# Kernel tuning notes

Hardware: AMD Instinct MI355X
Metric: run time of the kernel (lower is better)

Reference implementation:

```python
import jax, jax.numpy as jnp
import numpy as np

H = 16
D_MODEL = 1024
D_K = D_MODEL // H


def setup_inputs() -> dict:
    key = jax.random.key(0)
    ks = jax.random.split(key, 10)
    B, S = 2, 2048
    q = jax.random.normal(ks[0], (B, S, D_MODEL), dtype=jnp.float32)
    k = jax.random.normal(ks[1], (B, S, D_MODEL), dtype=jnp.float32)
    v = jax.random.normal(ks[2], (B, S, D_MODEL), dtype=jnp.float32)
    mask = jax.random.randint(ks[3], (B, 1, S), 0, 2, dtype=jnp.int32)
    s = 1.0 / np.sqrt(D_MODEL)
    w_q = jax.random.normal(ks[4], (D_MODEL, D_MODEL), dtype=jnp.float32) * s
    b_q = jnp.zeros((D_MODEL,), dtype=jnp.float32)
    w_v = jax.random.normal(ks[5], (D_MODEL, D_MODEL), dtype=jnp.float32) * s
    b_v = jnp.zeros((D_MODEL,), dtype=jnp.float32)
    w_o = jax.random.normal(ks[6], (D_MODEL, D_MODEL), dtype=jnp.float32) * s
    b_o = jnp.zeros((D_MODEL,), dtype=jnp.float32)
    return {"q": q, "k": k, "v": v, "mask": mask,
            "w_q": w_q, "b_q": b_q, "w_v": w_v, "b_v": b_v,
            "w_o": w_o, "b_o": b_o}


def _split_heads(x, B):
    # [B, S, D] -> [B, H, S, d_k]
    return x.reshape(B, -1, H, D_K).transpose(0, 2, 1, 3)


def reference(q, k, v, mask, w_q, b_q, w_v, b_v, w_o, b_o):
    B = q.shape[0]
    # NOTE: source uses w_q for BOTH q and k (w_k is dead code) — reproduced faithfully.
    qh = _split_heads(q @ w_q.T + b_q, B)
    kh = _split_heads(k @ w_q.T + b_q, B)
    vh = _split_heads(v @ w_v.T + b_v, B)
    scores = jnp.einsum('bhqd,bhkd->bhqk', qh, kh) * (1.0 / np.sqrt(D_K))
    # mask [B,1,S] -> unsqueeze(1) -> [B,1,1,S], broadcast over heads and query dim
    m = mask[:, None, :, :]
    scores = jnp.where(m == 0, -jnp.inf, scores)
    attn = jax.nn.softmax(scores, axis=-1)  # dropout is identity (eval / p=0)
    out = jnp.einsum('bhqk,bhkd->bhqd', attn, vh)
    out = out.transpose(0, 2, 1, 3).reshape(B, -1, D_MODEL)
    out = out @ w_o.T + b_o
    return out, attn
```

## Files before the change

kernel.cpp:

```cpp
#include <hip/hip_runtime.h>

#define S_LEN 2048
#define DMODEL 1024
#define NH 16
#define DK 64
#define BATCH 2
#define BS (BATCH * S_LEN)
#define KHALF 1024

typedef _Float16 f16;
typedef _Float16 f16x8 __attribute__((ext_vector_type(8)));
typedef _Float16 f16x4 __attribute__((ext_vector_type(4)));
typedef float f32x4 __attribute__((ext_vector_type(4)));

__device__ __forceinline__ f32x4 mfma16(f16x8 a, f16x8 b, f32x4 c) {
  return __builtin_amdgcn_mfma_f32_16x16x32_f16(a, b, c, 0, 0, 0);
}

__global__ __launch_bounds__(256) void cvt6(
    const float* __restrict__ a0, const float* __restrict__ a1,
    const float* __restrict__ a2, const float* __restrict__ a3,
    const float* __restrict__ a4, const float* __restrict__ a5,
    f16* __restrict__ d0, f16* __restrict__ d1, f16* __restrict__ d2,
    f16* __restrict__ d3, f16* __restrict__ d4, f16* __restrict__ d5) {
  const int y = blockIdx.y;
  const float* s;
  f16* d;
  switch (y) {
    case 0: s = a0; d = d0; break;
    case 1: s = a1; d = d1; break;
    case 2: s = a2; d = d2; break;
    case 3: s = a3; d = d3; break;
    case 4: s = a4; d = d4; break;
    default: s = a5; d = d5; break;
  }
  const int n = (y < 3) ? BS * DMODEL : DMODEL * DMODEL;
  const int idx = (blockIdx.x * 256 + threadIdx.x) * 4;
  if (idx >= n) return;
  const float4 v = *reinterpret_cast<const float4*>(&s[idx]);
  f16x4 h = {(f16)v.x, (f16)v.y, (f16)v.z, (f16)v.w};
  *reinterpret_cast<f16x4*>(&d[idx]) = h;
}

template <int MODE>
__device__ __forceinline__ void gemm_body16(const f16* __restrict__ A,
                                            const f16* __restrict__ W,
                                            const float* __restrict__ bias,
                                            void* __restrict__ outp, float scale,
                                            f16 (*As)[72], f16 (*Ws)[72]) {
  const int t = threadIdx.x;
  const int m0 = blockIdx.y * 128;
  const int n0 = blockIdx.x * 128;
  const int wave = t >> 6, lane = t & 63;
  const int wr = wave >> 1, wc = wave & 1;
  const int lcol = lane & 15, kq = lane >> 4;

  f32x4 acc[4][4];
  const f32x4 zero = {0.f, 0.f, 0.f, 0.f};
#pragma unroll
  for (int i = 0; i < 4; ++i)
#pragma unroll
    for (int j = 0; j < 4; ++j) acc[i][j] = zero;

  for (int k0 = 0; k0 < DMODEL; k0 += 64) {
#pragma unroll
    for (int i = 0; i < 4; ++i) {
      const int f = t + i * 256;
      const int r = f >> 3, c = (f & 7) << 3;
      *reinterpret_cast<f16x8*>(&As[r][c]) =
          *reinterpret_cast<const f16x8*>(&A[(size_t)(m0 + r) * DMODEL + k0 + c]);
      *reinterpret_cast<f16x8*>(&Ws[r][c]) =
          *reinterpret_cast<const f16x8*>(&W[(size_t)(n0 + r) * DMODEL + k0 + c]);
    }
    __syncthreads();
#pragma unroll
    for (int ks = 0; ks < 2; ++ks) {
      f16x8 af[4], bf[4];
#pragma unroll
      for (int fr = 0; fr < 4; ++fr)
        af[fr] = *reinterpret_cast<const f16x8*>(
            &As[wr * 64 + fr * 16 + lcol][ks * 32 + kq * 8]);
#pragma unroll
      for (int fc = 0; fc < 4; ++fc)
        bf[fc] = *reinterpret_cast<const f16x8*>(
            &Ws[wc * 64 + fc * 16 + lcol][ks * 32 + kq * 8]);
#pragma unroll
      for (int fr = 0; fr < 4; ++fr)
#pragma unroll
        for (int fc = 0; fc < 4; ++fc)
          acc[fr][fc] = mfma16(af[fr], bf[fc], acc[fr][fc]);
    }
    __syncthreads();
  }

#pragma unroll
  for (int fc = 0; fc < 4; ++fc) {
    const int gj = n0 + wc * 64 + fc * 16 + lcol;
    const float bv = bias[gj];
#pragma unroll
    for (int fr = 0; fr < 4; ++fr) {
#pragma unroll
      for (int r = 0; r < 4; ++r) {
        const int gi = m0 + wr * 64 + fr * 16 + kq * 4 + r;
        const float val = (acc[fr][fc][r] + bv) * scale;
        if constexpr (MODE == 0) {
          const int b = gi >> 11, s = gi & 2047, h = gj >> 6, dk = gj & 63;
          ((f16*)outp)[(((size_t)(b * NH + h) * S_LEN) + s) * DK + dk] = (f16)val;
        } else if constexpr (MODE == 1) {
          const int b = gi >> 11, s = gi & 2047, h = gj >> 6, dk = gj & 63;
          ((f16*)outp)[(((size_t)(b * NH + h) * DK) + dk) * S_LEN + s] = (f16)val;
        } else {
          ((float*)outp)[(size_t)gi * DMODEL + gj] = val;
        }
      }
    }
  }
}

__global__ __launch_bounds__(256, 3) void qkv_gemm(
    const f16* __restrict__ qf, const f16* __restrict__ kf,
    const f16* __restrict__ vf, const f16* __restrict__ wq,
    const float* __restrict__ b_q, const f16* __restrict__ wv,
    const float* __restrict__ b_v, f16* __restrict__ qh, f16* __restrict__ kh,
    f16* __restrict__ vhT) {
  __shared__ f16 As[128][72];
  __shared__ f16 Ws[128][72];
  if (blockIdx.z == 0)
    gemm_body16<0>(qf, wq, b_q, qh, 0.125f, As, Ws);
  else if (blockIdx.z == 1)
    gemm_body16<0>(kf, wq, b_q, kh, 1.0f, As, Ws);
  else
    gemm_body16<1>(vf, wv, b_v, vhT, 1.0f, As, Ws);
}

__global__ __launch_bounds__(256, 2) void gemm_out(const f16* __restrict__ A,
                                                   const f16* __restrict__ W,
                                                   const float* __restrict__ bias,
                                                   float* __restrict__ outp) {
  __shared__ f16 As[128][72];
  __shared__ f16 Ws[128][72];
  gemm_body16<2>(A, W, bias, outp, 1.0f, As, Ws);
}

__global__ __launch_bounds__(256, 4) void attn_fused(
    const f16* __restrict__ qh, const f16* __restrict__ kh,
    const f16* __restrict__ vhT, const int* __restrict__ mask,
    float* __restrict__ attn, f16* __restrict__ ctx) {
  __shared__ __align__(16) unsigned char smem[17920];
  const int t = threadIdx.x;
  const int bh = blockIdx.y, b = bh >> 4, h = bh & 15;
  const int i0 = blockIdx.x * 64;
  const int wave = t >> 6, lane = t & 63;
  const int rh = wave & 1, khf = wave >> 1;
  const int lcol = lane & 15, kq = lane >> 4;
  const int rbase = i0 + rh * 32;
  const int jbase = khf * KHALF;
  float (*Ost)[68] = reinterpret_cast<float(*)[68]>(smem);
  float* lred = reinterpret_cast<float*>(smem + 17408);

  const f16* Q = qh + (size_t)bh * S_LEN * DK;
  const f16* K = kh + (size_t)bh * S_LEN * DK;
  const f16* V = vhT + (size_t)bh * DK * S_LEN;
  const int* msk = mask + b * S_LEN;
  float* Sc = attn + (size_t)bh * S_LEN * S_LEN;

  f16x8 aq[2][2];
#pragma unroll
  for (int rt = 0; rt < 2; ++rt)
#pragma unroll
    for (int ks = 0; ks < 2; ++ks)
      aq[rt][ks] = *reinterpret_cast<const f16x8*>(
          &Q[(size_t)(rbase + rt * 16 + lcol) * DK + ks * 32 + kq * 8]);

  float l_acc[2] = {0.f, 0.f};
  f32x4 o[2][4];
  const f32x4 zero = {0.f, 0.f, 0.f, 0.f};
#pragma unroll
  for (int rt = 0; rt < 2; ++rt)
#pragma unroll
    for (int d = 0; d < 4; ++d) o[rt][d] = zero;

  for (int j0 = jbase; j0 < jbase + KHALF; j0 += 64) {
#pragma unroll
    for (int jh = 0; jh < 2; ++jh) {
      f16x8 ap[2];
#pragma unroll
      for (int jl = 0; jl < 2; ++jl) {
        const int jt = jh * 2 + jl;
        const f16* Krow = &K[(size_t)(j0 + jt * 16 + lcol) * DK + kq * 8];
        const f16x8 bk0 = *reinterpret_cast<const f16x8*>(Krow);
        const f16x8 bk1 = *reinterpret_cast<const f16x8*>(Krow + 32);
        const int4 m4 =
            *reinterpret_cast<const int4*>(&msk[j0 + jt * 16 + kq * 4]);
#pragma unroll
        for (int rt = 0; rt < 2; ++rt) {
          f32x4 c = zero;
          c = mfma16(bk0, aq[rt][0], c);
          c = mfma16(bk1, aq[rt][1], c);
          const float p0 = m4.x ? __expf(c[0]) : 0.f;
          const float p1 = m4.y ? __expf(c[1]) : 0.f;
          const float p2 = m4.z ? __expf(c[2]) : 0.f;
          const float p3 = m4.w ? __expf(c[3]) : 0.f;
          l_acc[rt] += (p0 + p1) + (p2 + p3);
          ap[rt][jl * 4 + 0] = (f16)p0;
          ap[rt][jl * 4 + 1] = (f16)p1;
          ap[rt][jl * 4 + 2] = (f16)p2;
          ap[rt][jl * 4 + 3] = (f16)p3;
        }
      }
#pragma unroll
      for (int d = 0; d < 4; ++d) {
        const f16* Vr =
            &V[(size_t)(d * 16 + lcol) * S_LEN + j0 + jh * 32 + kq * 4];
        const f16x4 v0 = *reinterpret_cast<const f16x4*>(Vr);
        const f16x4 v1 = *reinterpret_cast<const f16x4*>(Vr + 16);
        f16x8 bv;
        bv[0] = v0[0]; bv[1] = v0[1]; bv[2] = v0[2]; bv[3] = v0[3];
        bv[4] = v1[0]; bv[5] = v1[1]; bv[6] = v1[2]; bv[7] = v1[3];
#pragma unroll
        for (int rt = 0; rt < 2; ++rt) o[rt][d] = mfma16(ap[rt], bv, o[rt][d]);
      }
    }
  }

#pragma unroll
  for (int rt = 0; rt < 2; ++rt) {
    float es = l_acc[rt];
    es += __shfl_xor(es, 16);
    es += __shfl_xor(es, 32);
    l_acc[rt] = es;
  }

  if (kq == 0) {
#pragma unroll
    for (int rt = 0; rt < 2; ++rt)
      lred[khf * 64 + rh * 32 + rt * 16 + lcol] = l_acc[rt];
  }
  if (khf == 1) {
#pragma unroll
    for (int rt = 0; rt < 2; ++rt)
#pragma unroll
      for (int d = 0; d < 4; ++d)
#pragma unroll
        for (int r = 0; r < 4; ++r)
          Ost[rh * 32 + rt * 16 + kq * 4 + r][d * 16 + lcol] = o[rt][d][r];
  }
  __syncthreads();

  float ile[2][4];
  float il2[2];
#pragma unroll
  for (int rt = 0; rt < 2; ++rt) {
#pragma unroll
    for (int r = 0; r < 4; ++r) {
      const int rl = rh * 32 + rt * 16 + kq * 4 + r;
      ile[rt][r] = 1.0f / (lred[rl] + lred[64 + rl]);
    }
    const int rl2 = rh * 32 + rt * 16 + lcol;
    il2[rt] = 1.0f / (lred[rl2] + lred[64 + rl2]);
  }

  for (int j0 = jbase; j0 < jbase + KHALF; j0 += 64) {
#pragma unroll
    for (int jt = 0; jt < 4; ++jt) {
      const f16* Krow = &K[(size_t)(j0 + jt * 16 + lcol) * DK + kq * 8];
      const f16x8 bk0 = *reinterpret_cast<const f16x8*>(Krow);
      const f16x8 bk1 = *reinterpret_cast<const f16x8*>(Krow + 32);
      const int4 m4 =
          *reinterpret_cast<const int4*>(&msk[j0 + jt * 16 + kq * 4]);
#pragma unroll
      for (int rt = 0; rt < 2; ++rt) {
        f32x4 c = zero;
        c = mfma16(bk0, aq[rt][0], c);
        c = mfma16(bk1, aq[rt][1], c);
        float4 st;
        st.x = m4.x ? __expf(c[0]) * il2[rt] : 0.f;
        st.y = m4.y ? __expf(c[1]) * il2[rt] : 0.f;
        st.z = m4.z ? __expf(c[2]) * il2[rt] : 0.f;
        st.w = m4.w ? __expf(c[3]) * il2[rt] : 0.f;
        *reinterpret_cast<float4*>(
            &Sc[((size_t)(rbase + rt * 16 + lcol) << 11) + j0 + jt * 16 +
                kq * 4]) = st;
      }
    }
  }

  if (khf == 0) {
#pragma unroll
    for (int rt = 0; rt < 2; ++rt)
#pragma unroll
      for (int d = 0; d < 4; ++d) {
        const int dk = d * 16 + lcol;
#pragma unroll
        for (int r = 0; r < 4; ++r) {
          const int rl = rh * 32 + rt * 16 + kq * 4 + r;
          const float ov = o[rt][d][r] + Ost[rl][dk];
          const int s = rbase + rt * 16 + kq * 4 + r;
          ctx[(size_t)(b * S_LEN + s) * DMODEL + h * DK + dk] =
              (f16)(ov * ile[rt][r]);
        }
      }
  }
}

extern "C" void kernel_launch(void* const* d_in, const int* in_sizes, int n_in,
                              void* d_out, int out_size, void* d_ws, size_t ws_size,
                              hipStream_t stream) {
  const float* q = (const float*)d_in[0];
  const float* k = (const float*)d_in[1];
  const float* v = (const float*)d_in[2];
  const int* mask = (const int*)d_in[3];
  const float* w_q = (const float*)d_in[4];
  const float* b_q = (const float*)d_in[5];
  const float* w_v = (const float*)d_in[6];
  const float* b_v = (const float*)d_in[7];
  const float* w_o = (const float*)d_in[8];
  const float* b_o = (const float*)d_in[9];

  float* out = (float*)d_out;
  float* attn = out + (size_t)BS * DMODEL;

  f16* qf = (f16*)d_ws;
  f16* kf = qf + (size_t)BS * DMODEL;
  f16* vf = kf + (size_t)BS * DMODEL;
  f16* wqf = vf + (size_t)BS * DMODEL;
  f16* wvf = wqf + (size_t)DMODEL * DMODEL;
  f16* wof = wvf + (size_t)DMODEL * DMODEL;
  f16* qh = wof + (size_t)DMODEL * DMODEL;
  f16* kh = qh + (size_t)BS * DMODEL;
  f16* vhT = kh + (size_t)BS * DMODEL;
  f16* ctx = vhT + (size_t)BS * DMODEL;

  cvt6<<<dim3(4096, 6), 256, 0, stream>>>(q, k, v, w_q, w_v, w_o, qf, kf, vf,
                                          wqf, wvf, wof);
  qkv_gemm<<<dim3(8, 32, 3), 256, 0, stream>>>(qf, kf, vf, wqf, b_q, wvf, b_v,
                                               qh, kh, vhT);
  attn_fused<<<dim3(32, 32), 256, 0, stream>>>(qh, kh, vhT, mask, attn, ctx);
  gemm_out<<<dim3(8, 32), 256, 0, stream>>>(ctx, wof, b_o, out);
}
```

Baseline: 1.035 ms.

## Stage K and V tiles through LDS in the fused attention kernel

The attention kernel now loads each 64-key tile of K and V, for both key halves, cooperatively into shared memory, with barriers around each load. The waves then read their MFMA operands from LDS instead of each wave issuing its own strided global loads. This cuts redundant global/L2 traffic, since the two row-half waves share a tile, and replaces scattered V loads with coalesced ones. In exchange, LDS per block grows to 36 KB, barriers are added each iteration with no double buffering, and occupancy may fall.

```diff
diff --git a/kernel.cpp b/kernel.cpp
--- a/kernel.cpp
+++ b/kernel.cpp
@@ -146,7 +146,12 @@
     const f16* __restrict__ qh, const f16* __restrict__ kh,
     const f16* __restrict__ vhT, const int* __restrict__ mask,
     float* __restrict__ attn, f16* __restrict__ ctx) {
-  __shared__ __align__(16) unsigned char smem[17920];
+  __shared__ __align__(16) unsigned char smem[36864];
+  f16 (*Kt)[64][72] = reinterpret_cast<f16(*)[64][72]>(smem);
+  f16 (*Vt)[64][72] = reinterpret_cast<f16(*)[64][72]>(smem + 18432);
+  float (*Ost)[68] = reinterpret_cast<float(*)[68]>(smem + 18432);
+  float* lred = reinterpret_cast<float*>(smem + 18432 + 17408);
+
   const int t = threadIdx.x;
   const int bh = blockIdx.y, b = bh >> 4, h = bh & 15;
   const int i0 = blockIdx.x * 64;
@@ -155,8 +160,6 @@
   const int lcol = lane & 15, kq = lane >> 4;
   const int rbase = i0 + rh * 32;
   const int jbase = khf * KHALF;
-  float (*Ost)[68] = reinterpret_cast<float(*)[68]>(smem);
-  float* lred = reinterpret_cast<float*>(smem + 17408);
 
   const f16* Q = qh + (size_t)bh * S_LEN * DK;
   const f16* K = kh + (size_t)bh * S_LEN * DK;
@@ -180,18 +183,34 @@
 #pragma unroll
     for (int d = 0; d < 4; ++d) o[rt][d] = zero;
 
-  for (int j0 = jbase; j0 < jbase + KHALF; j0 += 64) {
+  for (int j0 = 0; j0 < KHALF; j0 += 64) {
+    __syncthreads();
+#pragma unroll
+    for (int hf = 0; hf < 2; ++hf)
+#pragma unroll
+      for (int i = 0; i < 2; ++i) {
+        const int ch = t + i * 256;
+        const int r = ch >> 3, c = (ch & 7) << 3;
+        *reinterpret_cast<f16x8*>(&Kt[hf][r][c]) =
+            *reinterpret_cast<const f16x8*>(
+                &K[(size_t)(hf * KHALF + j0 + r) * DK + c]);
+        *reinterpret_cast<f16x8*>(&Vt[hf][r][c]) =
+            *reinterpret_cast<const f16x8*>(
+                &V[(size_t)r * S_LEN + hf * KHALF + j0 + c]);
+      }
+    __syncthreads();
 #pragma unroll
     for (int jh = 0; jh < 2; ++jh) {
       f16x8 ap[2];
 #pragma unroll
       for (int jl = 0; jl < 2; ++jl) {
         const int jt = jh * 2 + jl;
-        const f16* Krow = &K[(size_t)(j0 + jt * 16 + lcol) * DK + kq * 8];
-        const f16x8 bk0 = *reinterpret_cast<const f16x8*>(Krow);
-        const f16x8 bk1 = *reinterpret_cast<const f16x8*>(Krow + 32);
-        const int4 m4 =
-            *reinterpret_cast<const int4*>(&msk[j0 + jt * 16 + kq * 4]);
+        const f16x8 bk0 =
+            *reinterpret_cast<const f16x8*>(&Kt[khf][jt * 16 + lcol][kq * 8]);
+        const f16x8 bk1 = *reinterpret_cast<const f16x8*>(
+            &Kt[khf][jt * 16 + lcol][kq * 8 + 32]);
+        const int4 m4 = *reinterpret_cast<const int4*>(
+            &msk[jbase + j0 + jt * 16 + kq * 4]);
 #pragma unroll
         for (int rt = 0; rt < 2; ++rt) {
           f32x4 c = zero;
@@ -210,8 +229,7 @@
       }
 #pragma unroll
       for (int d = 0; d < 4; ++d) {
-        const f16* Vr =
-            &V[(size_t)(d * 16 + lcol) * S_LEN + j0 + jh * 32 + kq * 4];
+        const f16* Vr = &Vt[khf][d * 16 + lcol][jh * 32 + kq * 4];
         const f16x4 v0 = *reinterpret_cast<const f16x4*>(Vr);
         const f16x4 v1 = *reinterpret_cast<const f16x4*>(Vr + 16);
         f16x8 bv;
@@ -231,6 +249,7 @@
     l_acc[rt] = es;
   }
 
+  __syncthreads();
   if (kq == 0) {
 #pragma unroll
     for (int rt = 0; rt < 2; ++rt)
@@ -260,14 +279,27 @@
     il2[rt] = 1.0f / (lred[rl2] + lred[64 + rl2]);
   }
 
-  for (int j0 = jbase; j0 < jbase + KHALF; j0 += 64) {
+  for (int j0 = 0; j0 < KHALF; j0 += 64) {
+    __syncthreads();
+#pragma unroll
+    for (int hf = 0; hf < 2; ++hf)
+#pragma unroll
+      for (int i = 0; i < 2; ++i) {
+        const int ch = t + i * 256;
+        const int r = ch >> 3, c = (ch & 7) << 3;
+        *reinterpret_cast<f16x8*>(&Kt[hf][r][c]) =
+            *reinterpret_cast<const f16x8*>(
+                &K[(size_t)(hf * KHALF + j0 + r) * DK + c]);
+      }
+    __syncthreads();
 #pragma unroll
     for (int jt = 0; jt < 4; ++jt) {
-      const f16* Krow = &K[(size_t)(j0 + jt * 16 + lcol) * DK + kq * 8];
-      const f16x8 bk0 = *reinterpret_cast<const f16x8*>(Krow);
-      const f16x8 bk1 = *reinterpret_cast<const f16x8*>(Krow + 32);
+      const f16x8 bk0 =
+          *reinterpret_cast<const f16x8*>(&Kt[khf][jt * 16 + lcol][kq * 8]);
+      const f16x8 bk1 = *reinterpret_cast<const f16x8*>(
+          &Kt[khf][jt * 16 + lcol][kq * 8 + 32]);
       const int4 m4 =
-          *reinterpret_cast<const int4*>(&msk[j0 + jt * 16 + kq * 4]);
+          *reinterpret_cast<const int4*>(&msk[jbase + j0 + jt * 16 + kq * 4]);
 #pragma unroll
       for (int rt = 0; rt < 2; ++rt) {
         f32x4 c = zero;
@@ -279,8 +311,8 @@
         st.z = m4.z ? __expf(c[2]) * il2[rt] : 0.f;
         st.w = m4.w ? __expf(c[3]) * il2[rt] : 0.f;
         *reinterpret_cast<float4*>(
-            &Sc[((size_t)(rbase + rt * 16 + lcol) << 11) + j0 + jt * 16 +
-                kq * 4]) = st;
+            &Sc[((size_t)(rbase + rt * 16 + lcol) << 11) + jbase + j0 +
+                jt * 16 + kq * 4]) = st;
       }
     }
   }
```

Result: faster. 919.4 us (-11.1%).
